# Optimization experiments

Measured on AMD Instinct MI355X. Metric: run time of the kernel, lower is better.

The kernel has to match this reference:

```python
import jax, jax.numpy as jnp
import numpy as np

B, C, H, W = 4, 256, 64, 64
Q = 150          # num_queries
HID = 1024       # q_after hidden size
NEG = 1e9


def setup_inputs() -> dict:
    key = jax.random.key(0)
    ks = jax.random.split(key, 12)
    img_feat = jax.random.normal(ks[0], (B, C, H, W), jnp.float32)
    exe_feat = jax.random.normal(ks[1], (B, C, 7, 7), jnp.float32)
    mask = jax.random.randint(ks[2], (B, H, W), 0, 2).astype(jnp.float32)
    # parameters (similarity init = identity + small noise for a non-degenerate test)
    S = jnp.eye(C, dtype=jnp.float32) + 0.02 * jax.random.normal(ks[3], (C, C), jnp.float32)
    Wv = jax.random.normal(ks[4], (C, C), jnp.float32) / np.sqrt(C)
    ln_g = jnp.ones((C + 1,), jnp.float32)
    ln_b = jnp.zeros((C + 1,), jnp.float32)
    W1 = jax.random.normal(ks[5], (HID, C + 1), jnp.float32) / np.sqrt(C + 1)
    b1 = jnp.zeros((HID,), jnp.float32)
    W2 = jax.random.normal(ks[6], (C + 1, HID), jnp.float32) / np.sqrt(HID)
    b2 = jnp.zeros((C + 1,), jnp.float32)
    return {"img_feat": img_feat, "exe_feat": exe_feat, "mask": mask, "S": S,
            "Wv": Wv, "ln_g": ln_g, "ln_b": ln_b, "W1": W1, "b1": b1, "W2": W2, "b2": b2}


def _get_queries(simil):
    # simil: [B,H,W] detached heatmap; local-maxima NMS then top-k
    c1 = simil[:, :-1] >= simil[:, 1:]
    c2 = simil[:, 1:] > simil[:, :-1]
    c3 = simil[:, :, :-1] >= simil[:, :, 1:]
    c4 = simil[:, :, 1:] > simil[:, :, :-1]
    interior = c1[:, 1:, 1:-1] & c2[:, :-1, 1:-1] & c3[:, 1:-1, 1:] & c4[:, 1:-1, :-1]
    is_max = jnp.zeros(simil.shape, bool).at[:, 1:-1, 1:-1].set(interior)
    sup = jnp.where(is_max, simil, simil - NEG)
    _, q_ids = jax.lax.top_k(sup.reshape(simil.shape[0], -1), Q)   # [B,Q]
    coords = jnp.stack([q_ids // W, q_ids % W], axis=2)            # [B,Q,2]
    return q_ids, coords


def _forward(img_feat, exe_feat, mask, S, Wv, ln_g, ln_b, W1, b1, W2, b2):
    b, c, h, w = img_feat.shape
    hw = h * w
    unrolled = img_feat.reshape(b, c, hw)                               # [B,C,HW]
    exe = exe_feat.mean(axis=(2, 3))[:, :, None]                        # [B,C,1]
    concat = jnp.concatenate([unrolled, exe], axis=2)                   # [B,C,HW+1]
    values = jnp.einsum('bcn,dc->bnd', concat, Wv)                      # [B,HW+1,C]
    attn = jnp.einsum('bcm,cd,bdn->bmn', unrolled, S, concat)           # [B,HW,HW+1]
    hm = attn[:, :, -1].reshape(b, 1, h, w)
    q_ids, coords = _get_queries(jax.lax.stop_gradient(attn[:, :, -1]).reshape(b, h, w))
    # mask bias: outer product of pixel mask, exemplar column always allowed
    m2 = mask.reshape(b, hw, 1) * mask.reshape(b, 1, hw)
    m2 = jnp.concatenate([m2, jnp.ones((b, hw, 1), m2.dtype)], axis=2)
    attn = attn - (m2 != 1).astype(attn.dtype) * NEG
    attn = jax.nn.softmax(attn, axis=2)
    new_img = jnp.einsum('bmn,bnd->bmd', attn, values)                  # [B,HW,C]
    img_out = new_img.transpose(0, 2, 1).reshape(b, c, h, w) + img_feat
    img_out = jnp.concatenate([img_out, hm], axis=1)                    # [B,C+1,H,W]
    # gather query vectors at NMS peak locations
    q = jnp.take_along_axis(img_out.reshape(b, c + 1, hw), q_ids[:, None, :], axis=2)
    q = q.transpose(0, 2, 1)                                            # [B,Q,C+1]
    # q_after: LayerNorm -> Linear(1024) -> ReLU -> Linear(C+1)
    mu = q.mean(-1, keepdims=True)
    var = ((q - mu) ** 2).mean(-1, keepdims=True)
    qn = (q - mu) / jnp.sqrt(var + 1e-5) * ln_g + ln_b
    q_out = jax.nn.relu(qn @ W1.T + b1) @ W2.T + b2
    return img_out, q_out, coords


def reference(img_feat, exe_feat, mask, S, Wv, ln_g, ln_b, W1, b1, W2, b2):
    return _forward(img_feat, exe_feat, mask, S, Wv, ln_g, ln_b, W1, b1, W2, b2)
```

## Files before the change

### kernel.cpp

```cpp
#include <hip/hip_runtime.h>
#include <hip/hip_bf16.h>
#include <stdint.h>

typedef unsigned short u16;
typedef unsigned int u32;
typedef unsigned long long u64;
typedef __attribute__((ext_vector_type(8))) unsigned short u16x8;
typedef __attribute__((ext_vector_type(8))) short short8;
typedef __attribute__((ext_vector_type(4))) float f32x4;

#define CB   4
#define CC   256
#define CHW  4096
#define CNQ  4097
#define NQP  150
#define CHID 1024
#define XTROWS 4160
#define VROW   4160

#define XT_OFF   0ul
#define VB_OFF   (XT_OFF  + (size_t)CB*XTROWS*CC*2)
#define ST_OFF   (VB_OFF  + (size_t)CB*CC*VROW*2)
#define EXE_OFF  (ST_OFF  + 131072ul)
#define ZL_OFF   (EXE_OFF + 4096ul)
#define HEAT_OFF (ZL_OFF  + 4096ul)
#define QID_OFF  (HEAT_OFF+ 65536ul)
#define W1T_OFF  (QID_OFF + 2560ul)
#define W2T_OFF  (W1T_OFF + 1052672ul)
#define HB_OFF   (W2T_OFF + 1052672ul)
#define QG_OFF   (HB_OFF  + 2457600ul)

__device__ __forceinline__ u16 f2b(float f){
  __hip_bfloat16 h = __float2bfloat16(f); u16 r; __builtin_memcpy(&r, &h, 2); return r;
}
__device__ __forceinline__ f32x4 mfma16(u16x8 a, u16x8 b, f32x4 c){
  short8 as, bs; __builtin_memcpy(&as, &a, 16); __builtin_memcpy(&bs, &b, 16);
  return __builtin_amdgcn_mfma_f32_16x16x32_bf16(as, bs, c, 0, 0, 0);
}
__device__ __forceinline__ u16x8 zero8(){
  u16x8 v;
  #pragma unroll
  for (int e = 0; e < 8; e++) v[e] = 0;
  return v;
}
__device__ __forceinline__ u16x8 cvt8(f32x4 a, f32x4 b){
  u16x8 v;
  v[0]=f2b(a[0]); v[1]=f2b(a[1]); v[2]=f2b(a[2]); v[3]=f2b(a[3]);
  v[4]=f2b(b[0]); v[5]=f2b(b[1]); v[6]=f2b(b[2]); v[7]=f2b(b[3]);
  return v;
}
__device__ __forceinline__ void glds16(const u16* gp, u16* lp){
  __builtin_amdgcn_global_load_lds(
      (const __attribute__((address_space(1))) u32*)gp,
      (__attribute__((address_space(3))) u32*)lp, 16, 0, 0);
}

__device__ __forceinline__ float dppx(float x, const int ctrl){
  return x;
}
#define DPPF(x, ctrl) __int_as_float(__builtin_amdgcn_mov_dpp(__float_as_int(x), (ctrl), 0xF, 0xF, true))
__device__ __forceinline__ float red16_max(float x){
  x = fmaxf(x, DPPF(x, 0xB1));
  x = fmaxf(x, DPPF(x, 0x4E));
  x = fmaxf(x, DPPF(x, 0x141));
  x = fmaxf(x, DPPF(x, 0x140));
  return x;
}
__device__ __forceinline__ float red16_sum(float x){
  x += DPPF(x, 0xB1);
  x += DPPF(x, 0x4E);
  x += DPPF(x, 0x141);
  x += DPPF(x, 0x140);
  return x;
}

__device__ __forceinline__ void tpose_body(const float* __restrict__ src,
    float* __restrict__ dst, int R, int C, int bx, int by, char* sbuf){
  float (*tile)[33] = (float(*)[33])sbuf;
  int c0 = bx*32, r0 = by*32;
  int tc = threadIdx.x & 31, tr = threadIdx.x >> 5;
  for (int i = tr; i < 32; i += 8){
    int r = r0 + i, c = c0 + tc;
    tile[i][tc] = (r < R && c < C) ? src[(long)r*C + c] : 0.f;
  }
  __syncthreads();
  for (int i = tr; i < 32; i += 8){
    int c = c0 + i, r = r0 + tc;
    if (c < C && r < R) dst[(long)c*R + r] = tile[tc][i];
  }
}

__device__ __forceinline__ void t64_body(const float* __restrict__ src,
    u16* __restrict__ dst, int srcLd, long srcBatch, int dstLd, long dstBatch,
    int swz, int bx, int by, int bz, char* sbuf){
  u16 (*tile)[72] = (u16(*)[72])sbuf;
  int c0 = bx*64, m0 = by*64;
  const float* S = src + (long)bz*srcBatch;
  u16* D = dst + (long)bz*dstBatch;
  int t = threadIdx.x;
  int r = t >> 2, q = t & 3;
  for (int uu = q; uu < 8; uu += 4){
    const float* p = S + (long)(c0+r)*srcLd + m0 + uu*8;
    f32x4 a0 = *(const f32x4*)p;
    f32x4 a1 = *(const f32x4*)(p + 4);
    *(u16x8*)&tile[r][uu*8] = cvt8(a0, a1);
  }
  __syncthreads();
  for (int uu = q; uu < 8; uu += 4){
    u16x8 v;
    #pragma unroll
    for (int e = 0; e < 8; e++) v[e] = tile[uu*8 + e][r];
    int gidx = (c0 >> 3) + uu;
    if (swz) gidx ^= (r & 7)*4;
    *(u16x8*)(D + (long)(m0+r)*dstLd + gidx*8) = v;
  }
}

__global__ __launch_bounds__(256) void prep_k(
    const float* __restrict__ exe, const float* __restrict__ S,
    const float* __restrict__ W1, const float* __restrict__ W2,
    float* __restrict__ exeF, float* __restrict__ zl, u16* __restrict__ Xt,
    u16* __restrict__ St, float* __restrict__ W1t, float* __restrict__ W2t){
  __shared__ __align__(16) char sbuf[9216];
  int id = blockIdx.x, t = threadIdx.x;
  if (id < 4){
    float* em = (float*)sbuf;
    int b = id;
    const float* p = exe + (b*CC + t)*49;
    float s = 0.f;
    for (int i = 0; i < 49; i++) s += p[i];
    float m = s / 49.f;
    em[t] = m;
    exeF[b*CC + t] = m;
    u16* xb = Xt + (size_t)b*XTROWS*CC;
    xb[(size_t)CHW*CC + t] = f2b(m);
    for (int i = 0; i < 63; i++)
      xb[(size_t)(CHW + 1 + i)*CC + t] = 0;
    __syncthreads();
    const float* Sr = S + (long)t*CC;
    float z = 0.f;
    for (int d = 0; d < CC; d++) z += Sr[d] * em[d];
    zl[b*CC + t] = z;
  } else if (id < 292){
    int i = id - 4;
    tpose_body(W1, W1t, CHID, 257, i % 9, i / 9, sbuf);
  } else if (id < 580){
    int i = id - 292;
    tpose_body(W2, W2t, 257, CHID, i % 32, i / 32, sbuf);
  } else {
    int i = id - 580;
    t64_body(S, St, CC, 0, CC, 0, 0, i & 3, i >> 2, 0, sbuf);
  }
}

__global__ __launch_bounds__(256) void big_k(
    const float* __restrict__ img, const float* __restrict__ exeF,
    const float* __restrict__ zl, u16* __restrict__ Xt, u16* __restrict__ Vb,
    float* __restrict__ heat, float* __restrict__ out_img){
  __shared__ __align__(16) char sbuf[9216];
  int id = blockIdx.x, t = threadIdx.x;
  if (id < 1024){
    int bx = id & 3, by = (id >> 2) & 63, bz = id >> 8;
    t64_body(img, Xt, CHW, (long)CC*CHW, CC, (long)XTROWS*CC, 1, bx, by, bz, sbuf);
  } else if (id < 2048){
    int rc = id - 1024;
    int c = rc & 255;
    const float* srcrow = img + (long)rc*CHW;
    u16* drow = Vb + (long)rc*VROW;
    int cx = c & 7;
    for (int grp = t; grp < VROW/8; grp += 256){
      int G = (grp & ~7) | ((grp & 7) ^ cx);
      int col0 = G*8;
      u16x8 v;
      if (col0 + 8 <= CHW){
        f32x4 a0 = *(const f32x4*)(srcrow + col0);
        f32x4 a1 = *(const f32x4*)(srcrow + col0 + 4);
        v = cvt8(a0, a1);
      } else {
        v = zero8();
        if (col0 == CHW) v[0] = f2b(exeF[rc]);
      }
      *(u16x8*)(drow + grp*8) = v;
    }
  } else {
    int i = id - 2048;
    int bx = i & 15, b = i >> 4;
    float* z = (float*)sbuf;
    z[t] = zl[b*CC + t];
    __syncthreads();
    int m = bx*256 + t;
    const float* base = img + (long)b*CC*CHW + m;
    float s = 0.f;
    for (int c = 0; c < CC; c++) s += base[(long)c*CHW] * z[c];
    heat[b*CHW + m] = s;
    out_img[(long)b*257*CHW + (long)256*CHW + m] = s;
  }
}

__global__ __launch_bounds__(1024) void topk_k(const float* __restrict__ heat,
                                               int* __restrict__ qids,
                                               float* __restrict__ out_coords){
  int b = blockIdx.x, t = threadIdx.x;
  __shared__ unsigned long long sk[4096];
  const float* hb = heat + (long)b*CHW;
  for (int p = t; p < 4096; p += 1024){
    int i = p >> 6, j = p & 63;
    float h = hb[p];
    bool ismax = false;
    if (i >= 1 && i < 63 && j >= 1 && j < 63){
      ismax = (h >= hb[p+64]) && (h > hb[p-64]) && (h >= hb[p+1]) && (h > hb[p-1]);
    }
    float sup = ismax ? h : (h - 1e9f);
    unsigned u = __float_as_uint(sup);
    u = (u & 0x80000000u) ? ~u : (u | 0x80000000u);
    unsigned long long key = ((unsigned long long)u << 32) | (unsigned)(0xFFFFFFFFu - (unsigned)p);
    sk[p] = ~key;
  }
  __syncthreads();
  for (int k = 2; k <= 4096; k <<= 1){
    for (int j = k >> 1; j > 0; j >>= 1){
      for (int tt = t; tt < 2048; tt += 1024){
        int i1 = 2*tt - (tt & (j-1));
        int i2 = i1 + j;
        unsigned long long a = sk[i1], c = sk[i2];
        bool up = ((i1 & k) == 0);
        if (up ? (a > c) : (a < c)){ sk[i1] = c; sk[i2] = a; }
      }
      __syncthreads();
    }
  }
  if (t < NQP){
    unsigned long long key = ~sk[t];
    int p = (int)(0xFFFFFFFFu - (unsigned)(key & 0xFFFFFFFFull));
    qids[b*160 + t] = p;
    out_coords[((long)b*NQP + t)*2 + 0] = (float)(p >> 6);
    out_coords[((long)b*NQP + t)*2 + 1] = (float)(p & 63);
  }
}

__global__ __launch_bounds__(512, 2) void flash_k(
    const u16* __restrict__ Xt, const u16* __restrict__ St,
    const u16* __restrict__ Vb, const float* __restrict__ imgf,
    const float* __restrict__ maskp, const float* __restrict__ Wv,
    float* __restrict__ out_img){
  __shared__ __align__(16) char smem[144384];
  u16*   kp0 = (u16*)smem;
  u16*   kt0 = (u16*)(smem + 32768);
  u16*   kp1 = (u16*)(smem + 65536);
  u16*   kt1 = (u16*)(smem + 98304);
  u16*   p_tile = (u16*)(smem + 131072);
  unsigned char* maskb = (unsigned char*)(smem + 139264);
  float* mlx = (float*)(smem + 143360);

  int b = blockIdx.y;
  int m0 = blockIdx.x*64;
  int t = threadIdx.x;
  int lane = t & 63, l15 = lane & 15, qd = lane >> 4;
  int w = t >> 6, wm = w & 3, wn = w >> 2;
  f32x4 zero4 = {0.f,0.f,0.f,0.f};

  {
    const float* mp = maskp + (long)b*CHW + t*8;
    f32x4 a0 = *(const f32x4*)mp;
    f32x4 a1 = *(const f32x4*)(mp + 4);
    unsigned long long pk = 0;
    #pragma unroll
    for (int e = 0; e < 4; e++){
      pk |= (unsigned long long)(a0[e] == 1.0f ? 1u : 0u) << (8*e);
      pk |= (unsigned long long)(a1[e] == 1.0f ? 1u : 0u) << (8*(e+4));
    }
    *(unsigned long long*)&maskb[t*8] = pk;
  }

  const u16* xtb = Xt + (size_t)b*XTROWS*CC;
  const u16* vbb = Vb + (size_t)b*CC*VROW;

  {
    f32x4 D[8];
    #pragma unroll
    for (int i = 0; i < 8; i++) D[i] = zero4;
    const u16* arow = xtb + (long)(m0 + wm*16 + l15)*CC;
    int rsw = (l15 & 7)*4;
    #pragma unroll
    for (int ks = 0; ks < 8; ks++){
      u16x8 af = *(const u16x8*)(arow + ((ks*4 + qd) ^ rsw)*8);
      #pragma unroll
      for (int ds = 0; ds < 8; ds++){
        int dsg = wn*8 + ds;
        u16x8 bf_ = *(const u16x8*)(St + (long)(dsg*16 + l15)*CC + ks*32 + qd*8);
        D[ds] = mfma16(af, bf_, D[ds]);
      }
    }
    #pragma unroll
    for (int ds = 0; ds < 8; ds++){
      #pragma unroll
      for (int r = 0; r < 4; r++){
        int prow = wm*16 + qd*4 + r;
        int ccol = (wn*8 + ds)*16 + l15;
        kp0[prow*256 + ((ccol >> 3) ^ ((prow & 7)*4))*8 + (ccol & 7)] = f2b(D[ds][r]);
      }
    }
  }
  __syncthreads();
  u16x8 afrag[8];
  {
    int arl = wm*16 + l15;
    #pragma unroll
    for (int ks = 0; ks < 8; ks++)
      afrag[ks] = *(const u16x8*)&kp0[arl*256 + (((ks*4 + qd)) ^ ((arl & 7)*4))*8];
  }
  int rowAllowed[4];
  float mi[4], li[4];
  #pragma unroll
  for (int r = 0; r < 4; r++){
    int m = m0 + wm*16 + qd*4 + r;
    rowAllowed[r] = maskb[m];
    mi[r] = -1e30f; li[r] = 0.f;
  }
  f32x4 O[16];
  #pragma unroll
  for (int i = 0; i < 16; i++) O[i] = zero4;
  __syncthreads();

  {
    const u16* ksrc = xtb + w*2048 + lane*8;
    u16* kl = kp0 + w*2048;
    glds16(ksrc,        kl);
    glds16(ksrc + 512,  kl + 512);
    glds16(ksrc + 1024, kl + 1024);
    glds16(ksrc + 1536, kl + 1536);
    const u16* vsrc = vbb + (long)(w*32 + (lane >> 3))*VROW + (lane & 7)*8;
    u16* vl = kt0 + w*2048;
    glds16(vsrc,            vl);
    glds16(vsrc + 8*VROW,   vl + 512);
    glds16(vsrc + 16*VROW,  vl + 1024);
    glds16(vsrc + 24*VROW,  vl + 1536);
  }
  __syncthreads();

  for (int nt = 0; nt < 65; nt++){
    int cur = nt & 1;
    const u16* kpc = cur ? kp1 : kp0;
    const u16* ktc = cur ? kt1 : kt0;
    u16* kpn = cur ? kp0 : kp1;
    u16* ktn = cur ? kt0 : kt1;
    int n0 = nt*64;

    if (nt < 64){
      int n1 = n0 + 64;
      const u16* ksrc = xtb + (long)n1*CC + w*2048 + lane*8;
      u16* kl = kpn + w*2048;
      glds16(ksrc,        kl);
      glds16(ksrc + 512,  kl + 512);
      glds16(ksrc + 1024, kl + 1024);
      glds16(ksrc + 1536, kl + 1536);
      const u16* vsrc = vbb + (long)(w*32 + (lane >> 3))*VROW + n1 + (lane & 7)*8;
      u16* vl = ktn + w*2048;
      glds16(vsrc,            vl);
      glds16(vsrc + 8*VROW,   vl + 512);
      glds16(vsrc + 16*VROW,  vl + 1024);
      glds16(vsrc + 24*VROW,  vl + 1536);
    }

    f32x4 sc[2];
    sc[0] = zero4; sc[1] = zero4;
    __builtin_amdgcn_s_setprio(1);
    #pragma unroll
    for (int ks = 0; ks < 8; ks++){
      #pragma unroll
      for (int ns = 0; ns < 2; ns++){
        int n_l = (wn*2 + ns)*16 + l15;
        u16x8 bfrag = *(const u16x8*)&kpc[n_l*256 + (((ks*4 + qd)) ^ ((n_l & 7)*4))*8];
        sc[ns] = mfma16(afrag[ks], bfrag, sc[ns]);
      }
    }
    __builtin_amdgcn_s_setprio(0);

    float sEff[2][4];
    #pragma unroll
    for (int ns = 0; ns < 2; ns++){
      int n = n0 + (wn*2 + ns)*16 + l15;
      bool inv = (n >= CNQ);
      bool isEx = (n == CHW);
      int cm = 0;
      if (!inv && !isEx) cm = maskb[n];
      #pragma unroll
      for (int r = 0; r < 4; r++){
        float s = sc[ns][r];
        float se;
        if (inv)        se = -1e30f;
        else if (isEx)  se = s;
        else            se = (rowAllowed[r] & cm) ? s : s - 1e9f;
        sEff[ns][r] = se;
      }
    }
    float al[4], nm[4];
    #pragma unroll
    for (int r = 0; r < 4; r++){
      float tm = red16_max(fmaxf(sEff[0][r], sEff[1][r]));
      float newm = fmaxf(mi[r], tm);
      al[r] = (mi[r] < -1e29f) ? 0.f : __expf(fmaxf(mi[r] - newm, -88.f));
      nm[r] = newm; mi[r] = newm;
    }
    #pragma unroll
    for (int r = 0; r < 4; r++){
      float rs = 0.f;
      int prow = wm*16 + qd*4 + r;
      #pragma unroll
      for (int ns = 0; ns < 2; ns++){
        float p = __expf(fmaxf(sEff[ns][r] - nm[r], -88.f));
        rs += p;
        int ccol = (wn*2 + ns)*16 + l15;
        p_tile[prow*64 + ((ccol >> 3) ^ (prow & 7))*8 + (ccol & 7)] = f2b(p);
      }
      li[r] = li[r]*al[r] + red16_sum(rs);
    }
    asm volatile("s_waitcnt lgkmcnt(0)" ::: "memory");

    int needre = (al[0] != 1.f) | (al[1] != 1.f) | (al[2] != 1.f) | (al[3] != 1.f);
    if (__any(needre)){
      #pragma unroll
      for (int ds = 0; ds < 16; ds++){
        #pragma unroll
        for (int r = 0; r < 4; r++) O[ds][r] *= al[r];
      }
    }
    {
      int prow2 = wm*16 + l15;
      u16x8 pf = *(const u16x8*)&p_tile[prow2*64 + (((wn*4 + qd)) ^ (prow2 & 7))*8];
      __builtin_amdgcn_s_setprio(1);
      #pragma unroll
      for (int ds = 0; ds < 16; ds++){
        int c = ds*16 + l15;
        u16x8 vf = *(const u16x8*)&ktc[c*64 + (((wn*4 + qd)) ^ (c & 7))*8];
        O[ds] = mfma16(pf, vf, O[ds]);
      }
      __builtin_amdgcn_s_setprio(0);
    }
    __syncthreads();
  }

  if (l15 == 0){
    #pragma unroll
    for (int r = 0; r < 4; r++){
      mlx[(((wm*2 + wn)*16) + qd*4 + r)*2 + 0] = mi[r];
      mlx[(((wm*2 + wn)*16) + qd*4 + r)*2 + 1] = li[r];
    }
  }
  __syncthreads();
  float alpha[4], linv[4];
  #pragma unroll
  for (int r = 0; r < 4; r++){
    float mo = mlx[(((wm*2 + (1 - wn))*16) + qd*4 + r)*2 + 0];
    float lo = mlx[(((wm*2 + (1 - wn))*16) + qd*4 + r)*2 + 1];
    float ms = fmaxf(mi[r], mo);
    float aS = (mi[r] < -1e29f) ? 0.f : __expf(mi[r] - ms);
    float aO = (mo    < -1e29f) ? 0.f : __expf(mo - ms);
    float ls = li[r]*aS + lo*aO;
    alpha[r] = aS;
    linv[r] = (ls > 0.f) ? (1.0f / ls) : 0.f;
  }
  float* Tsum = (float*)smem;
  if (wn == 1){
    #pragma unroll
    for (int ds = 0; ds < 16; ds++){
      #pragma unroll
      for (int r = 0; r < 4; r++)
        Tsum[(wm*16 + qd*4 + r)*256 + ds*16 + l15] = O[ds][r]*alpha[r];
    }
  }
  __syncthreads();
  if (wn == 0){
    #pragma unroll
    for (int ds = 0; ds < 16; ds++){
      #pragma unroll
      for (int r = 0; r < 4; r++)
        O[ds][r] = (O[ds][r]*alpha[r] + Tsum[(wm*16 + qd*4 + r)*256 + ds*16 + l15]) * linv[r];
    }
  }
  __syncthreads();
  if (wn == 0){
    #pragma unroll
    for (int ds = 0; ds < 16; ds++){
      #pragma unroll
      for (int r = 0; r < 4; r++){
        int prow = wm*16 + qd*4 + r;
        int ccol = ds*16 + l15;
        kp0[prow*256 + ((ccol >> 3) ^ ((prow & 7)*4))*8 + (ccol & 7)] = f2b(O[ds][r]);
      }
    }
  }
  __syncthreads();
  u16x8 tfrag[8];
  {
    int arl = wm*16 + l15;
    #pragma unroll
    for (int ks = 0; ks < 8; ks++)
      tfrag[ks] = *(const u16x8*)&kp0[arl*256 + (((ks*4 + qd)) ^ ((arl & 7)*4))*8];
  }
  f32x4 F[8];
  #pragma unroll
  for (int i = 0; i < 8; i++) F[i] = zero4;
  #pragma unroll
  for (int ks = 0; ks < 8; ks++){
    #pragma unroll
    for (int ds = 0; ds < 8; ds++){
      int dsg = wn*8 + ds;
      const float* wr = Wv + (long)(dsg*16 + l15)*CC + ks*32 + qd*8;
      f32x4 w0 = *(const f32x4*)wr;
      f32x4 w1 = *(const f32x4*)(wr + 4);
      F[ds] = mfma16(tfrag[ks], cvt8(w0, w1), F[ds]);
    }
  }

  float* oi = out_img + (long)b*257*CHW;
  const float* fi = imgf + (long)b*CC*CHW;
  int mb = m0 + wm*16 + qd*4;
  #pragma unroll
  for (int ds = 0; ds < 8; ds++){
    int d = (wn*8 + ds)*16 + l15;
    f32x4 ivals = *(const f32x4*)(fi + (long)d*CHW + mb);
    f32x4 ovals;
    #pragma unroll
    for (int r = 0; r < 4; r++) ovals[r] = F[ds][r] + ivals[r];
    *(f32x4*)(oi + (long)d*CHW + mb) = ovals;
  }
}

__global__ __launch_bounds__(256) void gather_k(const float* __restrict__ out_img,
    const int* __restrict__ qids, float* __restrict__ qg){
  int id = blockIdx.x;
  int b = id / NQP, q = id - b*NQP;
  int m = qids[b*160 + q];
  int t = threadIdx.x;
  const float* oib = out_img + (long)b*257*CHW + m;
  qg[(long)id*257 + t] = oib[(long)t*CHW];
  if (t == 0) qg[(long)id*257 + 256] = oib[(long)256*CHW];
}

__global__ __launch_bounds__(256) void qhead1_k(const float* __restrict__ qg,
    const float* __restrict__ g, const float* __restrict__ be,
    const float* __restrict__ W1t, const float* __restrict__ b1,
    float* __restrict__ Hb){
  int hc = blockIdx.x, rb = blockIdx.y;
  int t = threadIdx.x, lane = t & 63, wv = t >> 6;
  __shared__ __align__(16) float xl[4][260];
  {
    const float* row = qg + (long)(rb*4 + wv)*257;
    float v[4];
    #pragma unroll
    for (int j = 0; j < 4; j++) v[j] = row[lane + j*64];
    float v4 = (lane == 0) ? row[256] : 0.f;
    float s = v[0]+v[1]+v[2]+v[3]+v4;
    #pragma unroll
    for (int d = 1; d < 64; d <<= 1) s += __shfl_xor(s, d, 64);
    float mu = s / 257.f;
    float d4 = (lane == 0) ? (v4 - mu) : 0.f;
    float vs = d4*d4;
    #pragma unroll
    for (int j = 0; j < 4; j++){ float dd = v[j]-mu; vs += dd*dd; }
    #pragma unroll
    for (int d = 1; d < 64; d <<= 1) vs += __shfl_xor(vs, d, 64);
    float inv = 1.0f / sqrtf(vs/257.f + 1e-5f);
    #pragma unroll
    for (int j = 0; j < 4; j++)
      xl[wv][lane + j*64] = (v[j]-mu)*inv*g[lane + j*64] + be[lane + j*64];
    if (lane == 0) xl[wv][256] = d4*inv*g[256] + be[256];
  }
  __syncthreads();
  int h = hc*256 + t;
  float acc0=0.f, acc1=0.f, acc2=0.f, acc3=0.f;
  #pragma unroll 8
  for (int c = 0; c < 256; c++){
    float wv_ = W1t[(long)c*CHID + h];
    acc0 += wv_*xl[0][c]; acc1 += wv_*xl[1][c];
    acc2 += wv_*xl[2][c]; acc3 += wv_*xl[3][c];
  }
  {
    float wv_ = W1t[(long)256*CHID + h];
    acc0 += wv_*xl[0][256]; acc1 += wv_*xl[1][256];
    acc2 += wv_*xl[2][256]; acc3 += wv_*xl[3][256];
  }
  float bb = b1[h];
  float* hb = Hb + (long)rb*4*CHID + h;
  hb[0]       = fmaxf(acc0 + bb, 0.f);
  hb[CHID]    = fmaxf(acc1 + bb, 0.f);
  hb[2*CHID]  = fmaxf(acc2 + bb, 0.f);
  hb[3*CHID]  = fmaxf(acc3 + bb, 0.f);
}

__global__ __launch_bounds__(256) void qhead2_k(float* __restrict__ qbuf,
    const float* __restrict__ Hb, const float* __restrict__ W2t,
    const float* __restrict__ b2){
  int rb = blockIdx.x;
  int t = threadIdx.x, lane = t & 63, wv = t >> 6;
  __shared__ __align__(16) float hl[4][CHID];
  const float* hs = Hb + (long)rb*4*CHID;
  #pragma unroll
  for (int q = 0; q < 4; q++)
    *(f32x4*)&hl[q][t*4] = *(const f32x4*)&hs[(long)q*CHID + t*4];
  __syncthreads();
  float a0=0.f, a1=0.f, a2=0.f, a3=0.f;
  #pragma unroll 8
  for (int c = 0; c < CHID; c++){
    float wv_ = W2t[(long)c*257 + t];
    a0 += wv_*hl[0][c]; a1 += wv_*hl[1][c];
    a2 += wv_*hl[2][c]; a3 += wv_*hl[3][c];
  }
  float bb = b2[t];
  qbuf[(long)(rb*4 + 0)*257 + t] = a0 + bb;
  qbuf[(long)(rb*4 + 1)*257 + t] = a1 + bb;
  qbuf[(long)(rb*4 + 2)*257 + t] = a2 + bb;
  qbuf[(long)(rb*4 + 3)*257 + t] = a3 + bb;
  if (wv == 0){
    float p0=0.f, p1=0.f, p2=0.f, p3=0.f;
    #pragma unroll
    for (int k = 0; k < 16; k++){
      int c = lane*16 + k;
      float wv_ = W2t[(long)c*257 + 256];
      p0 += wv_*hl[0][c]; p1 += wv_*hl[1][c];
      p2 += wv_*hl[2][c]; p3 += wv_*hl[3][c];
    }
    #pragma unroll
    for (int d = 1; d < 64; d <<= 1){
      p0 += __shfl_xor(p0, d, 64); p1 += __shfl_xor(p1, d, 64);
      p2 += __shfl_xor(p2, d, 64); p3 += __shfl_xor(p3, d, 64);
    }
    if (lane == 0){
      float b256 = b2[256];
      qbuf[(long)(rb*4 + 0)*257 + 256] = p0 + b256;
      qbuf[(long)(rb*4 + 1)*257 + 256] = p1 + b256;
      qbuf[(long)(rb*4 + 2)*257 + 256] = p2 + b256;
      qbuf[(long)(rb*4 + 3)*257 + 256] = p3 + b256;
    }
  }
}

extern "C" void kernel_launch(void* const* d_in, const int* in_sizes, int n_in,
                              void* d_out, int out_size, void* d_ws, size_t ws_size,
                              hipStream_t stream){
  (void)out_size; (void)ws_size;
  int idxImg=-1, idxExe=-1, idxMask=-1, idxB1=-1;
  int idx65[2]={-1,-1}; int n65=0;
  int idx263[2]={-1,-1}; int n263=0;
  int idx257[3]={-1,-1,-1}; int n257=0;
  for (int i = 0; i < n_in; i++){
    int s = in_sizes[i];
    if      (s == 4194304) idxImg = i;
    else if (s == 50176)   idxExe = i;
    else if (s == 16384)   idxMask = i;
    else if (s == 1024)    idxB1 = i;
    else if (s == 65536)  { if (n65 < 2)  idx65[n65++] = i; }
    else if (s == 263168) { if (n263 < 2) idx263[n263++] = i; }
    else if (s == 257)    { if (n257 < 3) idx257[n257++] = i; }
  }
  const float* img  = (const float*)d_in[idxImg];
  const float* exe  = (const float*)d_in[idxExe];
  const float* mask = (const float*)d_in[idxMask];
  const float* S    = (const float*)d_in[idx65[0]];
  const float* Wv   = (const float*)d_in[idx65[1]];
  const float* W1   = (const float*)d_in[idx263[0]];
  const float* W2   = (const float*)d_in[idx263[1]];
  const float* b1   = (const float*)d_in[idxB1];
  const float *lng, *lnb, *b2;
  if (idxImg == 0){
    lng = (const float*)d_in[idx257[0]];
    lnb = (const float*)d_in[idx257[1]];
    b2  = (const float*)d_in[idx257[2]];
  } else {
    b2  = (const float*)d_in[idx257[0]];
    lnb = (const float*)d_in[idx257[1]];
    lng = (const float*)d_in[idx257[2]];
  }

  char* ws = (char*)d_ws;
  u16*   Xt   = (u16*)(ws + XT_OFF);
  u16*   Vb   = (u16*)(ws + VB_OFF);
  u16*   St   = (u16*)(ws + ST_OFF);
  float* exeF = (float*)(ws + EXE_OFF);
  float* zl   = (float*)(ws + ZL_OFF);
  float* heat = (float*)(ws + HEAT_OFF);
  int*   qids = (int*)(ws + QID_OFF);
  float* W1t  = (float*)(ws + W1T_OFF);
  float* W2t  = (float*)(ws + W2T_OFF);
  float* Hb   = (float*)(ws + HB_OFF);
  float* qg   = (float*)(ws + QG_OFF);

  float* out      = (float*)d_out;
  float* out_img  = out;
  float* qbuf     = out + (size_t)CB*257*CHW;
  float* out_crd  = qbuf + (size_t)CB*NQP*257;

  prep_k<<<dim3(596), dim3(256), 0, stream>>>(
      exe, S, W1, W2, exeF, zl, Xt, St, W1t, W2t);
  big_k<<<dim3(2112), dim3(256), 0, stream>>>(
      img, exeF, zl, Xt, Vb, heat, out_img);
  topk_k<<<dim3(CB), dim3(1024), 0, stream>>>(heat, qids, out_crd);
  flash_k<<<dim3(64, CB), dim3(512), 0, stream>>>(
      Xt, St, Vb, img, mask, Wv, out_img);
  gather_k<<<dim3(CB*NQP), dim3(256), 0, stream>>>(out_img, qids, qg);
  qhead1_k<<<dim3(4, CB*NQP/4), dim3(256), 0, stream>>>(
      qg, lng, lnb, W1t, b1, Hb);
  qhead2_k<<<dim3(CB*NQP/4), dim3(256), 0, stream>>>(qbuf, Hb, W2t, b2);
}
```

Baseline: 398.7 us.

## Merge prep, transpose, heatmap and top-k into one kernel; remap flash grid

Folds the prep, big and topk kernels into a single launch. Four blocks each compute the exemplar mean, the projection z, the full heatmap for one batch and the bitonic top-k in shared memory, while the other blocks do the transposes and bf16 conversions. The exemplar mean is recomputed in each block that needs it instead of being passed through global buffers. Flash_k moves to a 1D grid with an interleaved block-to-(batch,tile) mapping. The goal is to cut launch gaps and intermediate global traffic, at the risk that the four long serial heatmap/top-k blocks become the critical path of the merged kernel.

```diff
diff --git a/kernel.cpp b/kernel.cpp
--- a/kernel.cpp
+++ b/kernel.cpp
@@ -21,10 +21,7 @@
 #define XT_OFF   0ul
 #define VB_OFF   (XT_OFF  + (size_t)CB*XTROWS*CC*2)
 #define ST_OFF   (VB_OFF  + (size_t)CB*CC*VROW*2)
-#define EXE_OFF  (ST_OFF  + 131072ul)
-#define ZL_OFF   (EXE_OFF + 4096ul)
-#define HEAT_OFF (ZL_OFF  + 4096ul)
-#define QID_OFF  (HEAT_OFF+ 65536ul)
+#define QID_OFF  (ST_OFF  + 131072ul)
 #define W1T_OFF  (QID_OFF + 2560ul)
 #define W2T_OFF  (W1T_OFF + 1052672ul)
 #define HB_OFF   (W2T_OFF + 1052672ul)
@@ -55,9 +52,6 @@
       (__attribute__((address_space(3))) u32*)lp, 16, 0, 0);
 }
 
-__device__ __forceinline__ float dppx(float x, const int ctrl){
-  return x;
-}
 #define DPPF(x, ctrl) __int_as_float(__builtin_amdgcn_mov_dpp(__float_as_int(x), (ctrl), 0xF, 0xF, true))
 __device__ __forceinline__ float red16_max(float x){
   x = fmaxf(x, DPPF(x, 0xB1));
@@ -116,58 +110,113 @@
   }
 }
 
-__global__ __launch_bounds__(256) void prep_k(
+__global__ __launch_bounds__(256) void mega_k(
     const float* __restrict__ exe, const float* __restrict__ S,
     const float* __restrict__ W1, const float* __restrict__ W2,
-    float* __restrict__ exeF, float* __restrict__ zl, u16* __restrict__ Xt,
-    u16* __restrict__ St, float* __restrict__ W1t, float* __restrict__ W2t){
-  __shared__ __align__(16) char sbuf[9216];
+    const float* __restrict__ img,
+    u16* __restrict__ Xt, u16* __restrict__ St,
+    float* __restrict__ W1t, float* __restrict__ W2t, u16* __restrict__ Vb,
+    int* __restrict__ qids, float* __restrict__ out_coords,
+    float* __restrict__ out_img){
+  __shared__ __align__(16) char sbuf[51200];
   int id = blockIdx.x, t = threadIdx.x;
   if (id < 4){
-    float* em = (float*)sbuf;
+    float* hl = (float*)sbuf;
+    u64*   sk = (u64*)(sbuf + 16384);
+    float* em = (float*)(sbuf + 49152);
+    float* z  = (float*)(sbuf + 50176);
     int b = id;
+    {
+      const float* p = exe + (b*CC + t)*49;
+      float s = 0.f;
+      for (int i = 0; i < 49; i++) s += p[i];
+      em[t] = s / 49.f;
+    }
+    __syncthreads();
+    {
+      const float* Sr = S + (long)t*CC;
+      float s = 0.f;
+      for (int d = 0; d < CC; d++) s += Sr[d] * em[d];
+      z[t] = s;
+    }
+    __syncthreads();
+    for (int m = t; m < CHW; m += 256){
+      const float* base = img + (long)b*CC*CHW + m;
+      float s = 0.f;
+      for (int c = 0; c < CC; c++) s += base[(long)c*CHW] * z[c];
+      hl[m] = s;
+      out_img[(long)b*257*CHW + (long)256*CHW + m] = s;
+    }
+    __syncthreads();
+    for (int p = t; p < 4096; p += 256){
+      int i = p >> 6, j = p & 63;
+      float h = hl[p];
+      bool ismax = false;
+      if (i >= 1 && i < 63 && j >= 1 && j < 63){
+        ismax = (h >= hl[p+64]) && (h > hl[p-64]) && (h >= hl[p+1]) && (h > hl[p-1]);
+      }
+      float sup = ismax ? h : (h - 1e9f);
+      unsigned u = __float_as_uint(sup);
+      u = (u & 0x80000000u) ? ~u : (u | 0x80000000u);
+      u64 key = ((u64)u << 32) | (unsigned)(0xFFFFFFFFu - (unsigned)p);
+      sk[p] = ~key;
+    }
+    __syncthreads();
+    for (int k = 2; k <= 4096; k <<= 1){
+      for (int j = k >> 1; j > 0; j >>= 1){
+        for (int tt = t; tt < 2048; tt += 256){
+          int i1 = 2*tt - (tt & (j-1));
+          int i2 = i1 + j;
+          u64 a = sk[i1], c = sk[i2];
+          bool up = ((i1 & k) == 0);
+          if (up ? (a > c) : (a < c)){ sk[i1] = c; sk[i2] = a; }
+        }
+        __syncthreads();
+      }
+    }
+    if (t < NQP){
+      u64 key = ~sk[t];
+      int p = (int)(0xFFFFFFFFu - (unsigned)(key & 0xFFFFFFFFull));
+      qids[b*160 + t] = p;
+      out_coords[((long)b*NQP + t)*2 + 0] = (float)(p >> 6);
+      out_coords[((long)b*NQP + t)*2 + 1] = (float)(p & 63);
+    }
+  } else if (id < 8){
+    int b = id - 4;
     const float* p = exe + (b*CC + t)*49;
     float s = 0.f;
     for (int i = 0; i < 49; i++) s += p[i];
     float m = s / 49.f;
-    em[t] = m;
-    exeF[b*CC + t] = m;
     u16* xb = Xt + (size_t)b*XTROWS*CC;
     xb[(size_t)CHW*CC + t] = f2b(m);
     for (int i = 0; i < 63; i++)
       xb[(size_t)(CHW + 1 + i)*CC + t] = 0;
-    __syncthreads();
-    const float* Sr = S + (long)t*CC;
-    float z = 0.f;
-    for (int d = 0; d < CC; d++) z += Sr[d] * em[d];
-    zl[b*CC + t] = z;
-  } else if (id < 292){
-    int i = id - 4;
+  } else if (id < 296){
+    int i = id - 8;
     tpose_body(W1, W1t, CHID, 257, i % 9, i / 9, sbuf);
-  } else if (id < 580){
-    int i = id - 292;
+  } else if (id < 584){
+    int i = id - 296;
     tpose_body(W2, W2t, 257, CHID, i % 32, i / 32, sbuf);
+  } else if (id < 600){
+    int i = id - 584;
+    t64_body(S, St, CC, 0, CC, 0, 0, i & 3, i >> 2, 0, sbuf);
+  } else if (id < 1624){
+    int i = id - 600;
+    int bx = i & 3, by = (i >> 2) & 63, bz = i >> 8;
+    t64_body(img, Xt, CHW, (long)CC*CHW, CC, (long)XTROWS*CC, 1, bx, by, bz, sbuf);
   } else {
-    int i = id - 580;
-    t64_body(S, St, CC, 0, CC, 0, 0, i & 3, i >> 2, 0, sbuf);
-  }
-}
-
-__global__ __launch_bounds__(256) void big_k(
-    const float* __restrict__ img, const float* __restrict__ exeF,
-    const float* __restrict__ zl, u16* __restrict__ Xt, u16* __restrict__ Vb,
-    float* __restrict__ heat, float* __restrict__ out_img){
-  __shared__ __align__(16) char sbuf[9216];
-  int id = blockIdx.x, t = threadIdx.x;
-  if (id < 1024){
-    int bx = id & 3, by = (id >> 2) & 63, bz = id >> 8;
-    t64_body(img, Xt, CHW, (long)CC*CHW, CC, (long)XTROWS*CC, 1, bx, by, bz, sbuf);
-  } else if (id < 2048){
-    int rc = id - 1024;
+    int rc = id - 1624;
     int c = rc & 255;
     const float* srcrow = img + (long)rc*CHW;
     u16* drow = Vb + (long)rc*VROW;
     int cx = c & 7;
+    float exm = 0.f;
+    {
+      const float* p = exe + (long)rc*49;
+      float s = 0.f;
+      for (int i = 0; i < 49; i++) s += p[i];
+      exm = s / 49.f;
+    }
     for (int grp = t; grp < VROW/8; grp += 256){
       int G = (grp & ~7) | ((grp & 7) ^ cx);
       int col0 = G*8;
@@ -178,63 +227,10 @@
         v = cvt8(a0, a1);
       } else {
         v = zero8();
-        if (col0 == CHW) v[0] = f2b(exeF[rc]);
+        if (col0 == CHW) v[0] = f2b(exm);
       }
       *(u16x8*)(drow + grp*8) = v;
     }
-  } else {
-    int i = id - 2048;
-    int bx = i & 15, b = i >> 4;
-    float* z = (float*)sbuf;
-    z[t] = zl[b*CC + t];
-    __syncthreads();
-    int m = bx*256 + t;
-    const float* base = img + (long)b*CC*CHW + m;
-    float s = 0.f;
-    for (int c = 0; c < CC; c++) s += base[(long)c*CHW] * z[c];
-    heat[b*CHW + m] = s;
-    out_img[(long)b*257*CHW + (long)256*CHW + m] = s;
-  }
-}
-
-__global__ __launch_bounds__(1024) void topk_k(const float* __restrict__ heat,
-                                               int* __restrict__ qids,
-                                               float* __restrict__ out_coords){
-  int b = blockIdx.x, t = threadIdx.x;
-  __shared__ unsigned long long sk[4096];
-  const float* hb = heat + (long)b*CHW;
-  for (int p = t; p < 4096; p += 1024){
-    int i = p >> 6, j = p & 63;
-    float h = hb[p];
-    bool ismax = false;
-    if (i >= 1 && i < 63 && j >= 1 && j < 63){
-      ismax = (h >= hb[p+64]) && (h > hb[p-64]) && (h >= hb[p+1]) && (h > hb[p-1]);
-    }
-    float sup = ismax ? h : (h - 1e9f);
-    unsigned u = __float_as_uint(sup);
-    u = (u & 0x80000000u) ? ~u : (u | 0x80000000u);
-    unsigned long long key = ((unsigned long long)u << 32) | (unsigned)(0xFFFFFFFFu - (unsigned)p);
-    sk[p] = ~key;
-  }
-  __syncthreads();
-  for (int k = 2; k <= 4096; k <<= 1){
-    for (int j = k >> 1; j > 0; j >>= 1){
-      for (int tt = t; tt < 2048; tt += 1024){
-        int i1 = 2*tt - (tt & (j-1));
-        int i2 = i1 + j;
-        unsigned long long a = sk[i1], c = sk[i2];
-        bool up = ((i1 & k) == 0);
-        if (up ? (a > c) : (a < c)){ sk[i1] = c; sk[i2] = a; }
-      }
-      __syncthreads();
-    }
-  }
-  if (t < NQP){
-    unsigned long long key = ~sk[t];
-    int p = (int)(0xFFFFFFFFu - (unsigned)(key & 0xFFFFFFFFull));
-    qids[b*160 + t] = p;
-    out_coords[((long)b*NQP + t)*2 + 0] = (float)(p >> 6);
-    out_coords[((long)b*NQP + t)*2 + 1] = (float)(p & 63);
   }
 }
 
@@ -252,8 +248,10 @@
   unsigned char* maskb = (unsigned char*)(smem + 139264);
   float* mlx = (float*)(smem + 143360);
 
-  int b = blockIdx.y;
-  int m0 = blockIdx.x*64;
+  int f = blockIdx.x;
+  int l = (f & 7)*32 + (f >> 3);
+  int b = l >> 6;
+  int m0 = (l & 63)*64;
   int t = threadIdx.x;
   int lane = t & 63, l15 = lane & 15, qd = lane >> 4;
   int w = t >> 6, wm = w & 3, wn = w >> 2;
@@ -677,9 +675,6 @@
   u16*   Xt   = (u16*)(ws + XT_OFF);
   u16*   Vb   = (u16*)(ws + VB_OFF);
   u16*   St   = (u16*)(ws + ST_OFF);
-  float* exeF = (float*)(ws + EXE_OFF);
-  float* zl   = (float*)(ws + ZL_OFF);
-  float* heat = (float*)(ws + HEAT_OFF);
   int*   qids = (int*)(ws + QID_OFF);
   float* W1t  = (float*)(ws + W1T_OFF);
   float* W2t  = (float*)(ws + W2T_OFF);
@@ -691,12 +686,9 @@
   float* qbuf     = out + (size_t)CB*257*CHW;
   float* out_crd  = qbuf + (size_t)CB*NQP*257;
 
-  prep_k<<<dim3(596), dim3(256), 0, stream>>>(
-      exe, S, W1, W2, exeF, zl, Xt, St, W1t, W2t);
-  big_k<<<dim3(2112), dim3(256), 0, stream>>>(
-      img, exeF, zl, Xt, Vb, heat, out_img);
-  topk_k<<<dim3(CB), dim3(1024), 0, stream>>>(heat, qids, out_crd);
-  flash_k<<<dim3(64, CB), dim3(512), 0, stream>>>(
+  mega_k<<<dim3(2648), dim3(256), 0, stream>>>(
+      exe, S, W1, W2, img, Xt, St, W1t, W2t, Vb, qids, out_crd, out_img);
+  flash_k<<<dim3(256), dim3(512), 0, stream>>>(
       Xt, St, Vb, img, mask, Wv, out_img);
   gather_k<<<dim3(CB*NQP), dim3(256), 0, stream>>>(out_img, qids, qg);
   qhead1_k<<<dim3(4, CB*NQP/4), dim3(256), 0, stream>>>(
```

Result: slower. 552.2 us (+38.5%).
